# Optimization experiments

Hardware: AMD Instinct MI355X
Metric: run time of the kernel (lower is better)

Reference implementation:

```python
import jax, jax.numpy as jnp
import numpy as np

B, N, D = 2, 1024, 128
H = D // 2  # edge_importance hidden width


def setup_inputs() -> dict:
    key = jax.random.key(0)
    k0, k1, k2, k3, k4 = jax.random.split(key, 5)
    node_embeddings = jax.random.normal(k0, (B, N, D), dtype=jnp.float32)
    visited = jax.random.randint(k1, (B, N), 0, 2).astype(bool)
    remaining_capacity = jax.random.uniform(k2, (B, 1), dtype=jnp.float32)
    # edge_importance: Linear(2D -> H) -> ReLU -> Linear(H -> 1)
    W1 = jax.random.normal(k3, (H, 2 * D), dtype=jnp.float32) / np.sqrt(2 * D)
    b1 = jnp.zeros((H,), dtype=jnp.float32)
    W2 = jax.random.normal(k4, (1, H), dtype=jnp.float32) / np.sqrt(H)
    b2 = jnp.zeros((1,), dtype=jnp.float32)
    return {"node_embeddings": node_embeddings, "visited": visited,
            "remaining_capacity": remaining_capacity,
            "W1": W1, "b1": b1, "W2": W2, "b2": b2}


def reference(node_embeddings, visited, remaining_capacity, W1, b1, W2, b2):
    d = node_embeddings.shape[-1]
    # Linear on concat([node_i, node_j]) == split-weight sum; avoids the
    # [B,N,N,2D] concat while computing identical math.
    Wi, Wj = W1[:, :d], W1[:, d:]
    ai = jnp.einsum('bnd,hd->bnh', node_embeddings, Wi)  # [B,N,H]
    aj = jnp.einsum('bnd,hd->bnh', node_embeddings, Wj)  # [B,N,H]
    hidden = jax.nn.relu(ai[:, :, None, :] + aj[:, None, :, :] + b1)  # [B,N,N,H]
    edge_weights = jnp.einsum('bijh,oh->bij', hidden, W2) + b2[0]      # [B,N,N]
    visited_mask = visited[:, None, :] | visited[:, :, None]           # [B,N,N]
    edge_weights = jnp.where(visited_mask, jnp.float32(-1e9), edge_weights)
    adjacency = jax.nn.softmax(edge_weights, axis=-1)
    return adjacency
```

## Files before the change

### kernel.cpp

```cpp
#include <hip/hip_runtime.h>

#define Bb 2
#define Nn 1024
#define Dd 128
#define Hh 64

__global__ __launch_bounds__(256)
void k1_proj(const float* __restrict__ E, const float* __restrict__ W1,
             const float* __restrict__ b1, float* __restrict__ Pt,
             float* __restrict__ Qt) {
  __shared__ float El[64 * 129];
  __shared__ float Wl[128 * 33];

  const int t = threadIdx.x;
  const int oBase = blockIdx.x * 32;
  const int nBase = blockIdx.y * 64;
  const int b = blockIdx.z;

  const float* esrc = E + ((size_t)b * Nn + nBase) * Dd;
  #pragma unroll
  for (int k = 0; k < 8; ++k) {
    int q = t + k * 256;
    int n = q >> 5;
    int c = (q & 31) << 2;
    float4 v = *(const float4*)(esrc + n * Dd + c);
    float* dst = &El[n * 129 + c];
    dst[0] = v.x; dst[1] = v.y; dst[2] = v.z; dst[3] = v.w;
  }
  #pragma unroll
  for (int k = 0; k < 16; ++k) {
    int q = t + k * 256;
    int o = q >> 7;
    int d = q & 127;
    int oG = oBase + o;
    int src = (oG < Hh) ? (oG * 2 * Dd + d) : ((oG - Hh) * 2 * Dd + Dd + d);
    Wl[d * 33 + o] = W1[src];
  }
  __syncthreads();

  const int tn = t & 15;
  const int to = t >> 4;
  float acc[4][2] = {{0.f, 0.f}, {0.f, 0.f}, {0.f, 0.f}, {0.f, 0.f}};
  #pragma unroll 8
  for (int d = 0; d < 128; ++d) {
    float w0 = Wl[d * 33 + to * 2 + 0];
    float w1 = Wl[d * 33 + to * 2 + 1];
    #pragma unroll
    for (int a = 0; a < 4; ++a) {
      float e = El[(tn * 4 + a) * 129 + d];
      acc[a][0] = fmaf(e, w0, acc[a][0]);
      acc[a][1] = fmaf(e, w1, acc[a][1]);
    }
  }

  #pragma unroll
  for (int j = 0; j < 2; ++j) {
    int o = oBase + to * 2 + j;
    float4 v = make_float4(acc[0][j], acc[1][j], acc[2][j], acc[3][j]);
    float* dst;
    if (o < Hh) {
      float bias = b1[o];
      v.x += bias; v.y += bias; v.z += bias; v.w += bias;
      dst = Pt + ((size_t)b * Hh + o) * Nn + nBase + tn * 4;
    } else {
      dst = Qt + ((size_t)b * Hh + (o - Hh)) * Nn + nBase + tn * 4;
    }
    *(float4*)dst = v;
  }
}

__global__ __launch_bounds__(256)
void k2_edge(const float* __restrict__ Pt, const float* __restrict__ Qt,
             const float* __restrict__ W2, const float* __restrict__ b2,
             float* __restrict__ edge) {
  __shared__ float Pl[64 * 68];
  __shared__ float Ql[64 * 68];

  const int t = threadIdx.x;
  const int jBase = blockIdx.x * 64;
  const int iBase = blockIdx.y * 64;
  const int b = blockIdx.z;

  #pragma unroll
  for (int k = 0; k < 4; ++k) {
    int q = t + k * 256;
    int h = q >> 4;
    int c = (q & 15) << 2;
    float4 pv = *(const float4*)(Pt + ((size_t)b * Hh + h) * Nn + iBase + c);
    *(float4*)&Pl[h * 68 + c] = pv;
    float4 qv = *(const float4*)(Qt + ((size_t)b * Hh + h) * Nn + jBase + c);
    *(float4*)&Ql[h * 68 + c] = qv;
  }
  __syncthreads();

  const int tx = t & 15;
  const int ty = t >> 4;
  float acc[4][4] = {};
  #pragma unroll 4
  for (int h = 0; h < 64; ++h) {
    float w = W2[h];
    float4 pv = *(const float4*)&Pl[h * 68 + ty * 4];
    float4 qv = *(const float4*)&Ql[h * 68 + tx * 4];
    float p[4]  = {pv.x, pv.y, pv.z, pv.w};
    float qa[4] = {qv.x, qv.y, qv.z, qv.w};
    #pragma unroll
    for (int a = 0; a < 4; ++a)
      #pragma unroll
      for (int c = 0; c < 4; ++c)
        acc[a][c] = fmaf(w, fmaxf(p[a] + qa[c], 0.f), acc[a][c]);
  }

  const float b2v = b2[0];
  float* erow = edge + ((size_t)b * Nn + iBase + ty * 4) * Nn + jBase + tx * 4;
  #pragma unroll
  for (int a = 0; a < 4; ++a) {
    float4 v = make_float4(acc[a][0] + b2v, acc[a][1] + b2v,
                           acc[a][2] + b2v, acc[a][3] + b2v);
    *(float4*)(erow + (size_t)a * Nn) = v;
  }
}

__global__ __launch_bounds__(256)
void k3_softmax(float* __restrict__ out, const int* __restrict__ visited) {
  const int r = blockIdx.x;
  const int b = r >> 10;
  const int t = threadIdx.x;
  __shared__ float redm[4];
  __shared__ float reds[4];

  const bool vi = visited[r] != 0;
  float* row = out + (size_t)r * Nn;
  const int4 vj = *(const int4*)(visited + b * Nn + t * 4);
  const float4 ev = *(const float4*)(row + t * 4);

  const float NEG = -1000000000.0f;
  float v0 = (vi | (vj.x != 0)) ? NEG : ev.x;
  float v1 = (vi | (vj.y != 0)) ? NEG : ev.y;
  float v2 = (vi | (vj.z != 0)) ? NEG : ev.z;
  float v3 = (vi | (vj.w != 0)) ? NEG : ev.w;

  float m = fmaxf(fmaxf(v0, v1), fmaxf(v2, v3));
  #pragma unroll
  for (int off = 32; off > 0; off >>= 1)
    m = fmaxf(m, __shfl_xor(m, off));
  if ((t & 63) == 0) redm[t >> 6] = m;
  __syncthreads();
  m = fmaxf(fmaxf(redm[0], redm[1]), fmaxf(redm[2], redm[3]));

  float e0 = __expf(v0 - m), e1 = __expf(v1 - m);
  float e2 = __expf(v2 - m), e3 = __expf(v3 - m);
  float s = (e0 + e1) + (e2 + e3);
  #pragma unroll
  for (int off = 32; off > 0; off >>= 1)
    s += __shfl_xor(s, off);
  if ((t & 63) == 0) reds[t >> 6] = s;
  __syncthreads();
  s = (reds[0] + reds[1]) + (reds[2] + reds[3]);

  const float inv = 1.0f / s;
  *(float4*)(row + t * 4) = make_float4(e0 * inv, e1 * inv, e2 * inv, e3 * inv);
}

extern "C" void kernel_launch(void* const* d_in, const int* in_sizes, int n_in,
                              void* d_out, int out_size, void* d_ws, size_t ws_size,
                              hipStream_t stream) {
  const float* E       = (const float*)d_in[0];
  const int*   visited = (const int*)d_in[1];
  const float* W1      = (const float*)d_in[3];
  const float* b1      = (const float*)d_in[4];
  const float* W2      = (const float*)d_in[5];
  const float* b2      = (const float*)d_in[6];

  float* out = (float*)d_out;
  float* Pt  = (float*)d_ws;
  float* Qt  = (float*)((char*)d_ws + (size_t)Bb * Hh * Nn * sizeof(float));

  k1_proj<<<dim3(4, 16, Bb), 256, 0, stream>>>(E, W1, b1, Pt, Qt);
  k2_edge<<<dim3(16, 16, Bb), 256, 0, stream>>>(Pt, Qt, W2, b2, out);
  k3_softmax<<<dim3(Bb * Nn), 256, 0, stream>>>(out, visited);
}
```

Baseline: 91.93 us.

## Fold |W2| into projections, sort hidden units by sign, use packed FMA

The projection kernel now scales P and Q by |W2[h]| and reorders hidden units so the positive-weight ones come first. This works because relu(x)*w equals sign(w)*relu(|w|*x). The edge kernel can then replace the per-element multiply by W2 with a plain add or subtract over two ranges. It also uses packed 2-wide float ops and widens each block's j tile to 128 columns, so each thread computes 4x8 outputs. The projection kernel reads W1 straight from global memory as float4 instead of staging a transposed copy in LDS, and uses a swizzled LDS layout for E. The trade-offs are more registers and a changed rounding order.

Result: no change. 92.50 us (+0.6%).

```diff
diff --git a/kernel.cpp b/kernel.cpp
--- a/kernel.cpp
+++ b/kernel.cpp
@@ -5,12 +5,14 @@
 #define Dd 128
 #define Hh 64
 
+typedef float v2f __attribute__((ext_vector_type(2)));
+
+#define ELS 132
 __global__ __launch_bounds__(256)
 void k1_proj(const float* __restrict__ E, const float* __restrict__ W1,
-             const float* __restrict__ b1, float* __restrict__ Pt,
-             float* __restrict__ Qt) {
-  __shared__ float El[64 * 129];
-  __shared__ float Wl[128 * 33];
+             const float* __restrict__ b1, const float* __restrict__ W2,
+             float* __restrict__ Pt, float* __restrict__ Qt) {
+  __shared__ float El[64 * ELS];
 
   const int t = threadIdx.x;
   const int oBase = blockIdx.x * 32;
@@ -22,50 +24,65 @@
   for (int k = 0; k < 8; ++k) {
     int q = t + k * 256;
     int n = q >> 5;
-    int c = (q & 31) << 2;
-    float4 v = *(const float4*)(esrc + n * Dd + c);
-    float* dst = &El[n * 129 + c];
-    dst[0] = v.x; dst[1] = v.y; dst[2] = v.z; dst[3] = v.w;
-  }
-  #pragma unroll
-  for (int k = 0; k < 16; ++k) {
-    int q = t + k * 256;
-    int o = q >> 7;
-    int d = q & 127;
-    int oG = oBase + o;
-    int src = (oG < Hh) ? (oG * 2 * Dd + d) : ((oG - Hh) * 2 * Dd + Dd + d);
-    Wl[d * 33 + o] = W1[src];
+    int c4 = q & 31;
+    float4 v = *(const float4*)(esrc + n * Dd + (c4 << 2));
+    int pc = (c4 + (n >> 2)) & 31;
+    *(float4*)&El[n * ELS + (pc << 2)] = v;
   }
   __syncthreads();
 
   const int tn = t & 15;
   const int to = t >> 4;
-  float acc[4][2] = {{0.f, 0.f}, {0.f, 0.f}, {0.f, 0.f}, {0.f, 0.f}};
-  #pragma unroll 8
-  for (int d = 0; d < 128; ++d) {
-    float w0 = Wl[d * 33 + to * 2 + 0];
-    float w1 = Wl[d * 33 + to * 2 + 1];
+  const int o0 = oBase + to * 2;
+  const bool isP = (oBase < Hh);
+  const int h0 = isP ? o0 : (o0 - Hh);
+  const float* w0 = W1 + h0 * (2 * Dd) + (isP ? 0 : Dd);
+  const float* w1 = w0 + 2 * Dd;
+
+  v2f acc[4][2] = {};
+  const int rowb = 4 * tn * ELS;
+  #pragma unroll 4
+  for (int d = 0; d < 128; d += 4) {
+    int co = (((d >> 2) + tn) & 31) << 2;
+    float4 wa = *(const float4*)(w0 + d);
+    float4 wb = *(const float4*)(w1 + d);
+    v2f wa01 = {wa.x, wa.y}, wa23 = {wa.z, wa.w};
+    v2f wb01 = {wb.x, wb.y}, wb23 = {wb.z, wb.w};
     #pragma unroll
     for (int a = 0; a < 4; ++a) {
-      float e = El[(tn * 4 + a) * 129 + d];
-      acc[a][0] = fmaf(e, w0, acc[a][0]);
-      acc[a][1] = fmaf(e, w1, acc[a][1]);
-    }
-  }
-
-  #pragma unroll
-  for (int j = 0; j < 2; ++j) {
-    int o = oBase + to * 2 + j;
-    float4 v = make_float4(acc[0][j], acc[1][j], acc[2][j], acc[3][j]);
-    float* dst;
-    if (o < Hh) {
-      float bias = b1[o];
-      v.x += bias; v.y += bias; v.z += bias; v.w += bias;
-      dst = Pt + ((size_t)b * Hh + o) * Nn + nBase + tn * 4;
+      float4 e4 = *(const float4*)&El[rowb + a * ELS + co];
+      v2f e01 = {e4.x, e4.y}, e23 = {e4.z, e4.w};
+      acc[a][0] = __builtin_elementwise_fma(e01, wa01,
+                  __builtin_elementwise_fma(e23, wa23, acc[a][0]));
+      acc[a][1] = __builtin_elementwise_fma(e01, wb01,
+                  __builtin_elementwise_fma(e23, wb23, acc[a][1]));
+    }
+  }
+
+  unsigned long long mask = __ballot(W2[t & 63] >= 0.0f);
+  int nPos = __popcll(mask);
+
+  #pragma unroll
+  for (int oj = 0; oj < 2; ++oj) {
+    int h = h0 + oj;
+    float w2h = W2[h];
+    unsigned long long below = mask & ((1ull << h) - 1ull);
+    int nb = __popcll(below);
+    int row = (w2h >= 0.0f) ? nb : (nPos + (h - nb));
+    float s = fabsf(w2h);
+    float d0 = acc[0][oj].x + acc[0][oj].y;
+    float d1 = acc[1][oj].x + acc[1][oj].y;
+    float d2 = acc[2][oj].x + acc[2][oj].y;
+    float d3 = acc[3][oj].x + acc[3][oj].y;
+    float4 v;
+    if (isP) {
+      float bb = b1[h];
+      v = make_float4((d0 + bb) * s, (d1 + bb) * s, (d2 + bb) * s, (d3 + bb) * s);
     } else {
-      dst = Qt + ((size_t)b * Hh + (o - Hh)) * Nn + nBase + tn * 4;
-    }
-    *(float4*)dst = v;
+      v = make_float4(d0 * s, d1 * s, d2 * s, d3 * s);
+    }
+    float* base = isP ? Pt : Qt;
+    *(float4*)(base + ((size_t)b * Hh + row) * Nn + nBase + tn * 4) = v;
   }
 }
 
@@ -74,10 +91,10 @@
              const float* __restrict__ W2, const float* __restrict__ b2,
              float* __restrict__ edge) {
   __shared__ float Pl[64 * 68];
-  __shared__ float Ql[64 * 68];
+  __shared__ float Qs[2 * 64 * 68];
 
   const int t = threadIdx.x;
-  const int jBase = blockIdx.x * 64;
+  const int jBase = blockIdx.x * 128;
   const int iBase = blockIdx.y * 64;
   const int b = blockIdx.z;
 
@@ -86,37 +103,74 @@
     int q = t + k * 256;
     int h = q >> 4;
     int c = (q & 15) << 2;
-    float4 pv = *(const float4*)(Pt + ((size_t)b * Hh + h) * Nn + iBase + c);
-    *(float4*)&Pl[h * 68 + c] = pv;
-    float4 qv = *(const float4*)(Qt + ((size_t)b * Hh + h) * Nn + jBase + c);
-    *(float4*)&Ql[h * 68 + c] = qv;
-  }
+    *(float4*)&Pl[h * 68 + c] =
+        *(const float4*)(Pt + ((size_t)b * Hh + h) * Nn + iBase + c);
+  }
+  #pragma unroll
+  for (int k = 0; k < 8; ++k) {
+    int q = t + k * 256;
+    int h = q >> 5;
+    int c = (q & 31) << 2;
+    float4 v = *(const float4*)(Qt + ((size_t)b * Hh + h) * Nn + jBase + c);
+    int jq = c >> 3;
+    float* dst = &Qs[((c & 4) ? (64 * 68) : 0) + h * 68 + jq * 4];
+    *(float4*)dst = v;
+  }
+
+  unsigned long long mask = __ballot(W2[t & 63] >= 0.0f);
+  const int nPos = __popcll(mask);
   __syncthreads();
 
   const int tx = t & 15;
   const int ty = t >> 4;
-  float acc[4][4] = {};
+  const float* prow = &Pl[ty * 4];
+  const float* qrowA = &Qs[tx * 4];
+  const float* qrowB = qrowA + 64 * 68;
+
+  v2f acc[4][4] = {};
+  const v2f zero = {0.0f, 0.0f};
+  int h = 0;
   #pragma unroll 4
-  for (int h = 0; h < 64; ++h) {
-    float w = W2[h];
-    float4 pv = *(const float4*)&Pl[h * 68 + ty * 4];
-    float4 qv = *(const float4*)&Ql[h * 68 + tx * 4];
-    float p[4]  = {pv.x, pv.y, pv.z, pv.w};
-    float qa[4] = {qv.x, qv.y, qv.z, qv.w};
+  for (; h < nPos; ++h) {
+    float4 pv = *(const float4*)(prow + h * 68);
+    float4 qa = *(const float4*)(qrowA + h * 68);
+    float4 qb = *(const float4*)(qrowB + h * 68);
+    v2f qj[4] = {{qa.x, qa.y}, {qa.z, qa.w}, {qb.x, qb.y}, {qb.z, qb.w}};
+    float p[4] = {pv.x, pv.y, pv.z, pv.w};
     #pragma unroll
-    for (int a = 0; a < 4; ++a)
+    for (int a = 0; a < 4; ++a) {
+      v2f ps = {p[a], p[a]};
       #pragma unroll
       for (int c = 0; c < 4; ++c)
-        acc[a][c] = fmaf(w, fmaxf(p[a] + qa[c], 0.f), acc[a][c]);
+        acc[a][c] += __builtin_elementwise_max(ps + qj[c], zero);
+    }
+  }
+  #pragma unroll 4
+  for (; h < 64; ++h) {
+    float4 pv = *(const float4*)(prow + h * 68);
+    float4 qa = *(const float4*)(qrowA + h * 68);
+    float4 qb = *(const float4*)(qrowB + h * 68);
+    v2f qj[4] = {{qa.x, qa.y}, {qa.z, qa.w}, {qb.x, qb.y}, {qb.z, qb.w}};
+    float p[4] = {pv.x, pv.y, pv.z, pv.w};
+    #pragma unroll
+    for (int a = 0; a < 4; ++a) {
+      v2f ps = {p[a], p[a]};
+      #pragma unroll
+      for (int c = 0; c < 4; ++c)
+        acc[a][c] -= __builtin_elementwise_max(ps + qj[c], zero);
+    }
   }
 
   const float b2v = b2[0];
-  float* erow = edge + ((size_t)b * Nn + iBase + ty * 4) * Nn + jBase + tx * 4;
+  float* erow = edge + ((size_t)(b * Nn + iBase + ty * 4)) * Nn + jBase + tx * 8;
   #pragma unroll
   for (int a = 0; a < 4; ++a) {
-    float4 v = make_float4(acc[a][0] + b2v, acc[a][1] + b2v,
-                           acc[a][2] + b2v, acc[a][3] + b2v);
-    *(float4*)(erow + (size_t)a * Nn) = v;
+    float4 va = make_float4(acc[a][0].x + b2v, acc[a][0].y + b2v,
+                            acc[a][1].x + b2v, acc[a][1].y + b2v);
+    float4 vb = make_float4(acc[a][2].x + b2v, acc[a][2].y + b2v,
+                            acc[a][3].x + b2v, acc[a][3].y + b2v);
+    *(float4*)(erow + (size_t)a * Nn) = va;
+    *(float4*)(erow + (size_t)a * Nn + 4) = vb;
   }
 }
 
@@ -175,7 +229,7 @@
   float* Pt  = (float*)d_ws;
   float* Qt  = (float*)((char*)d_ws + (size_t)Bb * Hh * Nn * sizeof(float));
 
-  k1_proj<<<dim3(4, 16, Bb), 256, 0, stream>>>(E, W1, b1, Pt, Qt);
-  k2_edge<<<dim3(16, 16, Bb), 256, 0, stream>>>(Pt, Qt, W2, b2, out);
+  k1_proj<<<dim3(4, 16, Bb), 256, 0, stream>>>(E, W1, b1, W2, Pt, Qt);
+  k2_edge<<<dim3(8, 16, Bb), 256, 0, stream>>>(Pt, Qt, W2, b2, out);
   k3_softmax<<<dim3(Bb * Nn), 256, 0, stream>>>(out, visited);
 }
```
